# Optimization experiments

Hardware: AMD Instinct MI355X
Metric: run time of the kernel (lower is better)

Reference implementation:

```python
import jax, jax.numpy as jnp
import numpy as np

VOCAB = 50000
DIM = 50
B = 131072
CTX = 10
NEG = 10
EPS = 1e-10


def setup_inputs() -> dict:
    key = jax.random.key(0)
    k1, k2, k3, k4, k5 = jax.random.split(key, 5)
    return {
        "context_idxs": jax.random.randint(k1, (B, CTX), 0, VOCAB),
        "pos_target": jax.random.randint(k2, (B,), 0, VOCAB),
        "neg_samples": jax.random.randint(k3, (B, NEG), 0, VOCAB),
        "in_embed_W": jax.random.normal(k4, (VOCAB, DIM), dtype=jnp.float32),
        "out_embed_W": jax.random.normal(k5, (VOCAB, DIM), dtype=jnp.float32),
    }


def reference(context_idxs, pos_target, neg_samples, in_embed_W, out_embed_W):
    # context_vec: [B, D] = mean over context window of in_embed gathers
    context_vec = in_embed_W[context_idxs].mean(axis=1)
    # positive score: [B]
    pos_embeds = out_embed_W[pos_target]                      # [B, D]
    pos_score = jnp.sum(context_vec * pos_embeds, axis=1)     # [B]
    pos_loss = jnp.log(jax.nn.sigmoid(pos_score) + EPS)       # [B]
    # negative scores: [B, K] = bmm(neg_embeds [B,K,D], context_vec [B,D,1])
    neg_embeds = out_embed_W[neg_samples]                     # [B, K, D]
    neg_score = jnp.einsum("bkd,bd->bk", neg_embeds, context_vec)
    neg_loss = jnp.log(jax.nn.sigmoid(-neg_score) + EPS).sum(axis=1)  # [B]
    return -(pos_loss + neg_loss).mean()
```

## Files before the change

### kernel.cpp

```cpp
#include <hip/hip_runtime.h>
#include <hip/hip_fp8.h>

#define VOCAB 50000
#define DIM   50
#define B_TOT 131072
#define CTX   10
#define NEG   10
#define EPS_F 1e-10f
#define PAIRS (B_TOT / 2)

constexpr int TPB    = 256;
constexpr int BLOCKS = 4096;
constexpr int NWAVES = BLOCKS * (TPB / 64);
constexpr int ITERS  = PAIRS / NWAVES;
static_assert(PAIRS % NWAVES == 0, "exact division required");

constexpr size_t ROW8_B  = 64;
constexpr size_t TAB8_B  = (size_t)VOCAB * ROW8_B;
constexpr size_t WS_NEED = 2 * TAB8_B + BLOCKS * 4;

constexpr int BUF_W = 42 * 16;

typedef float vf2 __attribute__((ext_vector_type(2)));

static __device__ __forceinline__ void fp8x8_to_vf2x4(unsigned long long w,
                                                      vf2* f) {
#if __has_builtin(__builtin_amdgcn_cvt_pk_f32_fp8)
    const int lo = (int)(unsigned int)w;
    const int hi = (int)(unsigned int)(w >> 32);
    f[0] = __builtin_amdgcn_cvt_pk_f32_fp8(lo, false);
    f[1] = __builtin_amdgcn_cvt_pk_f32_fp8(lo, true);
    f[2] = __builtin_amdgcn_cvt_pk_f32_fp8(hi, false);
    f[3] = __builtin_amdgcn_cvt_pk_f32_fp8(hi, true);
#else
    #pragma unroll
    for (int i = 0; i < 4; ++i) {
        __hip_fp8_e4m3 a, b;
        a.__x = (unsigned char)(w >> (16 * i));
        b.__x = (unsigned char)(w >> (16 * i + 8));
        f[i][0] = (float)a;
        f[i][1] = (float)b;
    }
#endif
}

template <int CTRL>
static __device__ __forceinline__ float dpp_add(float x) {
    const int y = __builtin_amdgcn_mov_dpp(__float_as_int(x), CTRL, 0xF, 0xF, true);
    return x + __int_as_float(y);
}

__global__ __launch_bounds__(256) void cbow_convert(
    const float* __restrict__ inW, const float* __restrict__ outW,
    unsigned short* __restrict__ ws8)
{
    const int t = blockIdx.x * 256 + threadIdx.x;
    const int per_tab = VOCAB * 32;
    if (t >= 2 * per_tab) return;
    const int tab = t / per_tab;
    const int rem = t - tab * per_tab;
    const int r   = rem >> 5;
    const int j   = rem & 31;

    unsigned short u = 0;
    if (j < 25) {
        const float2* src2 = (const float2*)(tab ? outW : inW);
        const float2  v    = src2[r * 25 + j];
#if __has_builtin(__builtin_amdgcn_cvt_pk_fp8_f32)
        const int pk = __builtin_amdgcn_cvt_pk_fp8_f32(v.x, v.y, 0, false);
        u = (unsigned short)(pk & 0xffff);
#else
        __hip_fp8_e4m3 a(v.x), b(v.y);
        u = (unsigned short)(a.__x | (b.__x << 8));
#endif
    }
    ws8[(size_t)tab * (VOCAB * 32) + (size_t)r * 32 + j] = u;
}

__global__ __launch_bounds__(TPB, 7) void cbow_loss_fp8(
    const int* __restrict__ ctx_idx,
    const int* __restrict__ pos_idx,
    const int* __restrict__ neg_idx,
    const unsigned short* __restrict__ ws8,
    float* __restrict__ partials)
{
    __shared__ unsigned int lds[(TPB / 64) * 2 * BUF_W];

    const int lane = threadIdx.x & 63;
    const int sub  = lane >> 5;
    const int l    = lane & 31;
    const int quad = lane >> 2;
    const int qb   = (lane & 3) * 16;
    const int g    = (l >> 3) & 3;
    const int j    = l & 7;

    const int wave  = threadIdx.x >> 6;
    unsigned int* wbase = lds + wave * (2 * BUF_W);
    const int gwave = blockIdx.x * (TPB / 64) + wave;

    const char* in8  = (const char*)ws8;
    const char* out8 = (const char*)(ws8 + (size_t)VOCAB * 32);

    auto idx_addr = [&](int b) -> const int* {
        if (l < CTX)           return ctx_idx + b * CTX + l;
        if (l == CTX)          return pos_idx + b;
        if (l < CTX + 1 + NEG) return neg_idx + b * NEG + (l - CTX - 1);
        return pos_idx + b;
    };

    int my_idx[ITERS];
    #pragma unroll
    for (int i = 0; i < ITERS; ++i)
        my_idx[i] = *idx_addr(2 * (gwave + i * NWAVES) + sub);
    asm volatile("s_waitcnt vmcnt(0)" ::: "memory");

    auto issue = [&](unsigned int* dst, int midx) {
        #pragma unroll
        for (int t = 0; t < 3; ++t) {
            const int row  = t * 16 + quad;
            const int crow = (row > 41) ? 41 : row;
            const int sample = (crow >= 21) ? 1 : 0;
            const int slot   = crow - 21 * sample;
            const int idx = __shfl(midx, sample * 32 + slot);
            if (t < 2 || lane < 40) {
                const char* tb = (slot < CTX) ? in8 : out8;
                const char* ga = tb + ((size_t)(unsigned)idx << 6) + qb;
                __builtin_amdgcn_global_load_lds(
                    (const __attribute__((address_space(1))) unsigned int*)ga,
                    (__attribute__((address_space(3))) unsigned int*)(dst + t * 256),
                    16, 0, 0);
            }
        }
    };

    float loss_lane = 0.f;

    issue(wbase, my_idx[0]);

    #pragma unroll
    for (int i = 0; i < ITERS; ++i) {
        if (i + 1 < ITERS) {
            issue(wbase + ((i + 1) & 1) * BUF_W, my_idx[i + 1]);
            asm volatile("s_waitcnt vmcnt(3)" ::: "memory");
        } else {
            asm volatile("s_waitcnt vmcnt(0)" ::: "memory");
        }

        const unsigned int* buf = wbase + (i & 1) * BUF_W;
        const char* smp = (const char*)buf + sub * (21 * 64);

        vf2 cv[4] = {vf2{0.f, 0.f}, vf2{0.f, 0.f}, vf2{0.f, 0.f}, vf2{0.f, 0.f}};
        #pragma unroll
        for (int s = 0; s < 5; ++s) {
            const int r = (g & 1) * 5 + s;
            const unsigned long long w =
                *(const unsigned long long*)(smp + r * 64 + j * 8);
            vf2 f[4];
            fp8x8_to_vf2x4(w, f);
            #pragma unroll
            for (int d = 0; d < 4; ++d) cv[d] += f[d];
        }
        #pragma unroll
        for (int d = 0; d < 4; ++d) {
            cv[d][0] = dpp_add<0x128>(cv[d][0]);
            cv[d][1] = dpp_add<0x128>(cv[d][1]);
        }

        #pragma unroll
        for (int p = 0; p < 3; ++p) {
            int r = 10 + 4 * p + g;
            r = (r > 20) ? 20 : r;
            const unsigned long long w =
                *(const unsigned long long*)(smp + r * 64 + j * 8);
            vf2 f[4];
            fp8x8_to_vf2x4(w, f);
            vf2 acc2 = {0.f, 0.f};
            #pragma unroll
            for (int d = 0; d < 4; ++d) acc2 += cv[d] * f[d];
            float prod = acc2[0] + acc2[1];
            prod = dpp_add<0xB1>(prod);
            prod = dpp_add<0x4E>(prod);
            prod = dpp_add<0x141>(prod);

            const bool valid = (j == 0) && !(p == 2 && g == 3);
            const float sc   = prod * (1.f / CTX);
            const float z    = (p == 0 && g == 0) ? sc : -sc;
            const float c    = -__logf(1.f + __expf(-z));
            loss_lane += valid ? c : 0.f;
        }
    }

    loss_lane += __shfl_xor(loss_lane, 1);
    loss_lane += __shfl_xor(loss_lane, 2);
    loss_lane += __shfl_xor(loss_lane, 4);
    loss_lane += __shfl_xor(loss_lane, 8);
    loss_lane += __shfl_xor(loss_lane, 16);
    loss_lane += __shfl_xor(loss_lane, 32);

    __shared__ float s_part[TPB / 64];
    if (lane == 0) s_part[wave] = loss_lane;
    __syncthreads();
    if (threadIdx.x == 0) {
        float s = 0.f;
        #pragma unroll
        for (int w = 0; w < TPB / 64; ++w) s += s_part[w];
        partials[blockIdx.x] = s;
    }
}

__global__ __launch_bounds__(TPB) void cbow_loss_f32(
    const int*   __restrict__ ctx_idx, const int* __restrict__ pos_idx,
    const int*   __restrict__ neg_idx, const float* __restrict__ inW,
    const float* __restrict__ outW,    float* __restrict__ partials)
{
    const int lane = threadIdx.x & 63;
    const int sub  = lane >> 5;
    const int l    = lane & 31;
    const int p    = (l < 25) ? l : 24;
    const bool act = (l < 25);
    const int wave   = threadIdx.x >> 6;
    const int gwave  = blockIdx.x * (TPB / 64) + wave;
    const float2* inW2  = (const float2*)inW;
    const float2* outW2 = (const float2*)outW;

    float loss_lane = 0.f;
    for (int pair = gwave; pair < PAIRS; pair += NWAVES) {
        const int b = 2 * pair + sub;
        float cvx = 0.f, cvy = 0.f;
        #pragma unroll
        for (int jj = 0; jj < CTX; ++jj) {
            const float2 v = inW2[ctx_idx[b * CTX + jj] * 25 + p];
            cvx += v.x; cvy += v.y;
        }
        cvx *= (1.f / CTX); cvy *= (1.f / CTX);
        float packed = 0.f;
        #pragma unroll
        for (int r = 0; r <= NEG; ++r) {
            const int idx = (r == 0) ? pos_idx[b] : neg_idx[b * NEG + r - 1];
            const float2 v = outW2[idx * 25 + p];
            float prod = act ? (cvx * v.x + cvy * v.y) : 0.f;
            prod += __shfl_xor(prod, 1);
            prod += __shfl_xor(prod, 2);
            prod += __shfl_xor(prod, 4);
            prod += __shfl_xor(prod, 8);
            prod += __shfl_xor(prod, 16);
            packed = (l == r) ? prod : packed;
        }
        const float z   = (l == 0) ? packed : -packed;
        const float sig = 1.f / (1.f + __expf(-z));
        loss_lane += (l < NEG + 1) ? __logf(sig + EPS_F) : 0.f;
    }
    loss_lane += __shfl_xor(loss_lane, 1);
    loss_lane += __shfl_xor(loss_lane, 2);
    loss_lane += __shfl_xor(loss_lane, 4);
    loss_lane += __shfl_xor(loss_lane, 8);
    loss_lane += __shfl_xor(loss_lane, 16);
    loss_lane += __shfl_xor(loss_lane, 32);
    __shared__ float s_part[TPB / 64];
    if (lane == 0) s_part[wave] = loss_lane;
    __syncthreads();
    if (threadIdx.x == 0) {
        float s = 0.f;
        #pragma unroll
        for (int w = 0; w < TPB / 64; ++w) s += s_part[w];
        partials[blockIdx.x] = s;
    }
}

__global__ __launch_bounds__(256) void cbow_finalize(
    const float* __restrict__ partials, float* __restrict__ out)
{
    float s = 0.f;
    for (int i = threadIdx.x; i < BLOCKS; i += 256) s += partials[i];
    #pragma unroll
    for (int k = 32; k >= 1; k >>= 1) s += __shfl_xor(s, k);
    __shared__ float sm[4];
    const int w = threadIdx.x >> 6;
    if ((threadIdx.x & 63) == 0) sm[w] = s;
    __syncthreads();
    if (threadIdx.x == 0)
        out[0] = -(sm[0] + sm[1] + sm[2] + sm[3]) * (1.f / (float)B_TOT);
}

extern "C" void kernel_launch(void* const* d_in, const int* in_sizes, int n_in,
                              void* d_out, int out_size, void* d_ws, size_t ws_size,
                              hipStream_t stream) {
    const int*   ctx_idx = (const int*)  d_in[0];
    const int*   pos_idx = (const int*)  d_in[1];
    const int*   neg_idx = (const int*)  d_in[2];
    const float* inW     = (const float*)d_in[3];
    const float* outW    = (const float*)d_in[4];
    float*       out     = (float*)d_out;

    if (ws_size >= WS_NEED) {
        unsigned short* ws8 = (unsigned short*)d_ws;
        float* partials = (float*)((char*)d_ws + 2 * TAB8_B);
        const int conv_threads = 2 * VOCAB * 32;
        cbow_convert<<<(conv_threads + 255) / 256, 256, 0, stream>>>(inW, outW, ws8);
        cbow_loss_fp8<<<BLOCKS, TPB, 0, stream>>>(ctx_idx, pos_idx, neg_idx, ws8, partials);
        cbow_finalize<<<1, 256, 0, stream>>>(partials, out);
    } else {
        float* partials = (float*)d_ws;
        cbow_loss_f32<<<BLOCKS, TPB, 0, stream>>>(ctx_idx, pos_idx, neg_idx, inW, outW, partials);
        cbow_finalize<<<1, 256, 0, stream>>>(partials, out);
    }
}
```

Measured before the change: 111.0 us.

## Split per-iteration gather into separate context and output-table phases

Each wave's pipeline runs as two phases. The first phase gathers only in-embedding rows, reduces them to context vectors and stashes those in LDS. The second phase gathers only out-embedding rows for the positive and negative scores. This shrinks each double-buffer stage, lowers block LDS use and keeps each phase's gathers on a single table, which may help cache locality. In exchange it doubles the number of pipeline steps, each with less work to hide latency, and adds an LDS round-trip for the context vectors.

```diff
diff --git a/kernel.cpp b/kernel.cpp
--- a/kernel.cpp
+++ b/kernel.cpp
@@ -19,7 +19,9 @@
 constexpr size_t TAB8_B  = (size_t)VOCAB * ROW8_B;
 constexpr size_t WS_NEED = 2 * TAB8_B + BLOCKS * 4;
 
-constexpr int BUF_W = 42 * 16;
+constexpr int BUF_W  = 22 * 16;
+constexpr int CTX_W  = ITERS * 2 * 64;
+constexpr int WAVE_W = 2 * BUF_W + CTX_W;
 
 typedef float vf2 __attribute__((ext_vector_type(2)));
 
@@ -84,7 +86,7 @@
     const unsigned short* __restrict__ ws8,
     float* __restrict__ partials)
 {
-    __shared__ unsigned int lds[(TPB / 64) * 2 * BUF_W];
+    __shared__ unsigned int lds[(TPB / 64) * WAVE_W];
 
     const int lane = threadIdx.x & 63;
     const int sub  = lane >> 5;
@@ -95,7 +97,8 @@
     const int j    = l & 7;
 
     const int wave  = threadIdx.x >> 6;
-    unsigned int* wbase = lds + wave * (2 * BUF_W);
+    unsigned int* wbase = lds + wave * WAVE_W;
+    char* cbase = (char*)(wbase + 2 * BUF_W);
     const int gwave = blockIdx.x * (TPB / 64) + wave;
 
     const char* in8  = (const char*)ws8;
@@ -114,17 +117,16 @@
         my_idx[i] = *idx_addr(2 * (gwave + i * NWAVES) + sub);
     asm volatile("s_waitcnt vmcnt(0)" ::: "memory");
 
-    auto issue = [&](unsigned int* dst, int midx) {
-        #pragma unroll
-        for (int t = 0; t < 3; ++t) {
+    auto issueA = [&](unsigned int* dst, int midx) {
+        #pragma unroll
+        for (int t = 0; t < 2; ++t) {
             const int row  = t * 16 + quad;
-            const int crow = (row > 41) ? 41 : row;
-            const int sample = (crow >= 21) ? 1 : 0;
-            const int slot   = crow - 21 * sample;
+            const int crow = (row > 19) ? 19 : row;
+            const int sample = (crow >= 10) ? 1 : 0;
+            const int slot   = crow - 10 * sample;
             const int idx = __shfl(midx, sample * 32 + slot);
-            if (t < 2 || lane < 40) {
-                const char* tb = (slot < CTX) ? in8 : out8;
-                const char* ga = tb + ((size_t)(unsigned)idx << 6) + qb;
+            if (t == 0 || lane < 16) {
+                const char* ga = in8 + ((size_t)(unsigned)idx << 6) + qb;
                 __builtin_amdgcn_global_load_lds(
                     (const __attribute__((address_space(1))) unsigned int*)ga,
                     (__attribute__((address_space(3))) unsigned int*)(dst + t * 256),
@@ -133,60 +135,96 @@
         }
     };
 
+    auto issueB = [&](unsigned int* dst, int midx) {
+        #pragma unroll
+        for (int t = 0; t < 2; ++t) {
+            const int row  = t * 16 + quad;
+            const int crow = (row > 21) ? 21 : row;
+            const int sample = (crow >= 11) ? 1 : 0;
+            const int slot   = crow - 11 * sample;
+            const int idx = __shfl(midx, sample * 32 + CTX + slot);
+            if (t == 0 || lane < 24) {
+                const char* ga = out8 + ((size_t)(unsigned)idx << 6) + qb;
+                __builtin_amdgcn_global_load_lds(
+                    (const __attribute__((address_space(1))) unsigned int*)ga,
+                    (__attribute__((address_space(3))) unsigned int*)(dst + t * 256),
+                    16, 0, 0);
+            }
+        }
+    };
+
     float loss_lane = 0.f;
 
-    issue(wbase, my_idx[0]);
+    issueA(wbase, my_idx[0]);
 
     #pragma unroll
-    for (int i = 0; i < ITERS; ++i) {
-        if (i + 1 < ITERS) {
-            issue(wbase + ((i + 1) & 1) * BUF_W, my_idx[i + 1]);
-            asm volatile("s_waitcnt vmcnt(3)" ::: "memory");
+    for (int t = 0; t < 2 * ITERS; ++t) {
+        if (t + 1 < 2 * ITERS) {
+            unsigned int* nb = wbase + ((t + 1) & 1) * BUF_W;
+            if (t + 1 < ITERS) issueA(nb, my_idx[t + 1]);
+            else               issueB(nb, my_idx[t + 1 - ITERS]);
+            asm volatile("s_waitcnt vmcnt(2)" ::: "memory");
         } else {
             asm volatile("s_waitcnt vmcnt(0)" ::: "memory");
         }
 
-        const unsigned int* buf = wbase + (i & 1) * BUF_W;
-        const char* smp = (const char*)buf + sub * (21 * 64);
-
-        vf2 cv[4] = {vf2{0.f, 0.f}, vf2{0.f, 0.f}, vf2{0.f, 0.f}, vf2{0.f, 0.f}};
-        #pragma unroll
-        for (int s = 0; s < 5; ++s) {
-            const int r = (g & 1) * 5 + s;
-            const unsigned long long w =
-                *(const unsigned long long*)(smp + r * 64 + j * 8);
-            vf2 f[4];
-            fp8x8_to_vf2x4(w, f);
+        const unsigned int* buf = wbase + (t & 1) * BUF_W;
+
+        if (t < ITERS) {
+            const char* smp = (const char*)buf + sub * (10 * 64);
+            vf2 cv[4] = {vf2{0.f, 0.f}, vf2{0.f, 0.f}, vf2{0.f, 0.f}, vf2{0.f, 0.f}};
             #pragma unroll
-            for (int d = 0; d < 4; ++d) cv[d] += f[d];
-        }
-        #pragma unroll
-        for (int d = 0; d < 4; ++d) {
-            cv[d][0] = dpp_add<0x128>(cv[d][0]);
-            cv[d][1] = dpp_add<0x128>(cv[d][1]);
-        }
-
-        #pragma unroll
-        for (int p = 0; p < 3; ++p) {
-            int r = 10 + 4 * p + g;
-            r = (r > 20) ? 20 : r;
-            const unsigned long long w =
-                *(const unsigned long long*)(smp + r * 64 + j * 8);
-            vf2 f[4];
-            fp8x8_to_vf2x4(w, f);
-            vf2 acc2 = {0.f, 0.f};
+            for (int s = 0; s < 5; ++s) {
+                const int r = (g & 1) * 5 + s;
+                const unsigned long long w =
+                    *(const unsigned long long*)(smp + r * 64 + j * 8);
+                vf2 f[4];
+                fp8x8_to_vf2x4(w, f);
+                #pragma unroll
+                for (int d = 0; d < 4; ++d) cv[d] += f[d];
+            }
             #pragma unroll
-            for (int d = 0; d < 4; ++d) acc2 += cv[d] * f[d];
-            float prod = acc2[0] + acc2[1];
-            prod = dpp_add<0xB1>(prod);
-            prod = dpp_add<0x4E>(prod);
-            prod = dpp_add<0x141>(prod);
-
-            const bool valid = (j == 0) && !(p == 2 && g == 3);
-            const float sc   = prod * (1.f / CTX);
-            const float z    = (p == 0 && g == 0) ? sc : -sc;
-            const float c    = -__logf(1.f + __expf(-z));
-            loss_lane += valid ? c : 0.f;
+            for (int d = 0; d < 4; ++d) {
+                cv[d][0] = dpp_add<0x128>(cv[d][0]);
+                cv[d][1] = dpp_add<0x128>(cv[d][1]);
+            }
+            if ((l >> 3) == 0) {
+                float4* cd = (float4*)(cbase + t * 512 + sub * 256 + j * 32);
+                cd[0] = float4{cv[0][0], cv[0][1], cv[1][0], cv[1][1]};
+                cd[1] = float4{cv[2][0], cv[2][1], cv[3][0], cv[3][1]};
+            }
+        } else {
+            const int i = t - ITERS;
+            const float4* cs = (const float4*)(cbase + i * 512 + sub * 256 + j * 32);
+            const float4 c0 = cs[0];
+            const float4 c1 = cs[1];
+            vf2 cv[4];
+            cv[0] = vf2{c0.x, c0.y}; cv[1] = vf2{c0.z, c0.w};
+            cv[2] = vf2{c1.x, c1.y}; cv[3] = vf2{c1.z, c1.w};
+
+            const char* smp = (const char*)buf + sub * (11 * 64);
+            #pragma unroll
+            for (int p = 0; p < 3; ++p) {
+                int r = 4 * p + g;
+                r = (r > 10) ? 10 : r;
+                const unsigned long long w =
+                    *(const unsigned long long*)(smp + r * 64 + j * 8);
+                vf2 f[4];
+                fp8x8_to_vf2x4(w, f);
+                vf2 acc2 = {0.f, 0.f};
+                #pragma unroll
+                for (int d = 0; d < 4; ++d) acc2 += cv[d] * f[d];
+                float prod = acc2[0] + acc2[1];
+                prod = dpp_add<0xB1>(prod);
+                prod = dpp_add<0x4E>(prod);
+                prod = dpp_add<0x141>(prod);
+
+                const bool valid = (j == 0) && !(p == 2 && g == 3);
+                const float sc   = prod * (1.f / CTX);
+                const float z    = (p == 0 && g == 0) ? sc : -sc;
+                const float c    = -__logf(1.f + __expf(-z));
+                loss_lane += valid ? c : 0.f;
+            }
         }
     }
 
```

After: 113.4 us. 1.02x slower.
